# Performance work log

Measured on AMD Instinct MI355X. Metric: run time of the kernel, lower is better.

The kernel has to match this reference:

```python
import jax, jax.numpy as jnp
import numpy as np

N_NODES = 100000
N_EDGES = 1600000
N_GRAPHS = 1000


def _gcn_layer(x, W, b, row, col, dinv):
    # GCNConv with improved=True: A_hat = A + 2I, symmetric normalization.
    xw = x @ W  # [N, out]
    norm = dinv[row] * dinv[col]  # [E]
    agg = jax.ops.segment_sum(norm[:, None] * xw[row], col, num_segments=N_NODES)
    # self-loop contribution with fill weight 2.0
    agg = agg + (2.0 * dinv * dinv)[:, None] * xw
    return agg + b


def setup_inputs() -> dict:
    key = jax.random.key(0)
    ks = jax.random.split(key, 20)
    x = jax.random.normal(ks[0], (N_NODES, 336), dtype=jnp.float32)
    edge_index = jax.random.randint(ks[1], (2, N_EDGES), 0, N_NODES, dtype=jnp.int64)
    batch = jnp.sort(jax.random.randint(ks[2], (N_NODES,), 0, N_GRAPHS, dtype=jnp.int64))
    def lin(k, din, dout):
        s = 1.0 / np.sqrt(din)
        return jax.random.uniform(k, (din, dout), jnp.float32, -s, s)
    params = {
        'W1': lin(ks[3], 336, 100), 'b1': jnp.zeros((100,), jnp.float32),
        'W2': lin(ks[4], 100, 100), 'b2': jnp.zeros((100,), jnp.float32),
        'W3': lin(ks[5], 100, 100), 'b3': jnp.zeros((100,), jnp.float32),
        'W4': lin(ks[6], 100, 100), 'b4': jnp.zeros((100,), jnp.float32),
        'W5': lin(ks[7], 100, 100), 'b5': jnp.zeros((100,), jnp.float32),
        'Wl1': lin(ks[8], 100, 100), 'bl1': jnp.zeros((100,), jnp.float32),
        'Wl2': lin(ks[9], 100, 100), 'bl2': jnp.zeros((100,), jnp.float32),
        'Wl3': lin(ks[10], 100, 29), 'bl3': jnp.zeros((29,), jnp.float32),
    }
    return {'x': x, 'edge_index': edge_index, 'batch': batch, **params}


def reference(x, edge_index, batch, W1, b1, W2, b2, W3, b3, W4, b4, W5, b5,
              Wl1, bl1, Wl2, bl2, Wl3, bl3):
    row, col = edge_index[0], edge_index[1]
    # degree of A + 2I (edge weights are 1, self-loop weight 2)
    deg = jax.ops.segment_sum(jnp.ones((N_EDGES,), x.dtype), col, num_segments=N_NODES) + 2.0
    dinv = deg ** -0.5
    h = jax.nn.relu(_gcn_layer(x, W1, b1, row, col, dinv))
    h = jax.nn.relu(_gcn_layer(h, W2, b2, row, col, dinv))
    h = jax.nn.relu(_gcn_layer(h, W3, b3, row, col, dinv))
    h = jax.nn.relu(_gcn_layer(h, W4, b4, row, col, dinv))
    h = jax.nn.relu(_gcn_layer(h, W5, b5, row, col, dinv))
    # global mean pool over graphs
    sums = jax.ops.segment_sum(h, batch, num_segments=N_GRAPHS)
    counts = jax.ops.segment_sum(jnp.ones((N_NODES,), h.dtype), batch, num_segments=N_GRAPHS)
    pooled = sums / jnp.maximum(counts, 1.0)[:, None]
    g = jax.nn.relu(pooled @ Wl1 + bl1)
    g = jax.nn.relu(g @ Wl2 + bl2)
    return g @ Wl3 + bl3
```

## Files before the change

kernel.cpp:

```cpp
#include <hip/hip_runtime.h>
#include <hip/hip_fp16.h>
#include <stdint.h>

#define NN 100000
#define NE 1600000
#define NG 1000
#define LDA 112
#define LDX 128

#define NPART 8
#define PRANGE 12500
#define SGRID 2048
#define PSTRIDE 65536

typedef float f32x4 __attribute__((ext_vector_type(4)));
typedef _Float16 f16x8 __attribute__((ext_vector_type(8)));

__device__ __forceinline__ void load_lds16(const void* g, void* l) {
    __builtin_amdgcn_global_load_lds((const __attribute__((address_space(1))) unsigned int*)g,
                                     (__attribute__((address_space(3))) unsigned int*)l,
                                     16, 0, 0);
}

__global__ void k_deg(const int* __restrict__ col, int* __restrict__ degcnt) {
    int part = blockIdx.x & (NPART - 1);
    int pb = blockIdx.x >> 3;
    int lo = part * PRANGE, hi = lo + PRANGE;
    for (int e = pb * 256 + threadIdx.x; e < NE; e += PSTRIDE) {
        int c = col[e];
        if (c >= lo && c < hi) atomicAdd(&degcnt[c], 1);
    }
}

__global__ void k_scan1(const int* __restrict__ cnt, int* __restrict__ csum) {
    __shared__ int s[256];
    int i = blockIdx.x * 256 + threadIdx.x;
    s[threadIdx.x] = (i < NN) ? cnt[i] : 0;
    __syncthreads();
    for (int o = 128; o > 0; o >>= 1) {
        if (threadIdx.x < o) s[threadIdx.x] += s[threadIdx.x + o];
        __syncthreads();
    }
    if (threadIdx.x == 0) csum[blockIdx.x] = s[0];
}

__global__ void k_scan2(const int* __restrict__ csum, int* __restrict__ csum2, int nb) {
    __shared__ int s[512];
    int t = threadIdx.x;
    int v = (t < nb) ? csum[t] : 0;
    s[t] = v; __syncthreads();
    for (int o = 1; o < 512; o <<= 1) {
        int x = (t >= o) ? s[t - o] : 0;
        __syncthreads();
        s[t] += x;
        __syncthreads();
    }
    if (t < nb) csum2[t] = s[t] - v;
}

__global__ void k_scan3d(const int* __restrict__ cnt, const int* __restrict__ csum2,
                         int* __restrict__ indptr, float* __restrict__ dinv) {
    __shared__ int s[256];
    int t = threadIdx.x;
    int i = blockIdx.x * 256 + t;
    int v = (i < NN) ? cnt[i] : 0;
    s[t] = v; __syncthreads();
    for (int o = 1; o < 256; o <<= 1) {
        int x = (t >= o) ? s[t - o] : 0;
        __syncthreads();
        s[t] += x;
        __syncthreads();
    }
    if (i < NN) {
        indptr[i] = csum2[blockIdx.x] + s[t] - v;
        dinv[i] = 1.0f / sqrtf((float)v + 2.0f);
    }
    if (i == 0) indptr[NN] = NE;
}

__global__ void k_scatter(const int* __restrict__ row, const int* __restrict__ col,
                          const int* __restrict__ indptr,
                          int* __restrict__ fill, int* __restrict__ esrc) {
    int part = blockIdx.x & (NPART - 1);
    int pb = blockIdx.x >> 3;
    int lo = part * PRANGE, hi = lo + PRANGE;
    for (int e = pb * 256 + threadIdx.x; e < NE; e += PSTRIDE) {
        int c = col[e];
        int r = row[e];
        if (c >= lo && c < hi) {
            int pos = indptr[c] + atomicAdd(&fill[c], 1);
            esrc[pos] = r;
        }
    }
}

__global__ void k_gbounds(const int* __restrict__ batch, int* __restrict__ gstart) {
    int i = blockIdx.x * 256 + threadIdx.x;
    if (i >= NN) return;
    int b = batch[i];
    int pb = (i == 0) ? -1 : batch[i - 1];
    for (int g = pb + 1; g <= b; g++) gstart[g] = i;
    if (i == NN - 1) {
        for (int g = b + 1; g <= NG; g++) gstart[g] = NN;
    }
}

__global__ void k_convW(const float* __restrict__ W1, __half* __restrict__ w1h, __half* __restrict__ w1l,
                        const float* __restrict__ W2, __half* __restrict__ w2h, __half* __restrict__ w2l,
                        const float* __restrict__ W3, __half* __restrict__ w3h, __half* __restrict__ w3l,
                        const float* __restrict__ W4, __half* __restrict__ w4h, __half* __restrict__ w4l,
                        const float* __restrict__ W5, __half* __restrict__ w5h, __half* __restrict__ w5l) {
    int b = blockIdx.x, t = threadIdx.x;
    const float* W; __half *Wh, *Wl; int K, KCP, idx;
    if (b < 168) {
        W = W1; Wh = w1h; Wl = w1l; K = 336; KCP = 384; idx = b * 256 + t;
    } else {
        int li = (b - 168) / 56;
        int lb = (b - 168) % 56;
        const float* Ws[4] = {W2, W3, W4, W5};
        __half* Whs[4] = {w2h, w3h, w4h, w5h};
        __half* Wls[4] = {w2l, w3l, w4l, w5l};
        W = Ws[li]; Wh = Whs[li]; Wl = Wls[li]; K = 100; KCP = 128; idx = lb * 256 + t;
    }
    int n = idx / KCP, k = idx - n * KCP;
    float v = (n < 100 && k < K) ? W[k * 100 + n] : 0.f;
    __half hi = __float2half(v);
    __half lo = __float2half((v - __half2float(hi)) * 2048.f);
    int kc = k & 127;
    size_t so = (size_t)n * KCP + (k - kc) + (kc ^ ((n & 7) << 3));
    Wh[so] = hi;
    Wl[so] = lo;
}

__device__ __forceinline__ f16x8 cvt8(float4 v0, float4 v1) {
    __half2 p0 = __floats2half2_rn(v0.x, v0.y);
    __half2 p1 = __floats2half2_rn(v0.z, v0.w);
    __half2 p2 = __floats2half2_rn(v1.x, v1.y);
    __half2 p3 = __floats2half2_rn(v1.z, v1.w);
    union { uint4 u; f16x8 f; } c;
    c.u.x = __builtin_bit_cast(unsigned, p0);
    c.u.y = __builtin_bit_cast(unsigned, p1);
    c.u.z = __builtin_bit_cast(unsigned, p2);
    c.u.w = __builtin_bit_cast(unsigned, p3);
    return c.f;
}

__global__ __launch_bounds__(512, 4) void k_gemmX(const float* __restrict__ x,
                                                  const __half* __restrict__ Whi,
                                                  const __half* __restrict__ Wlo,
                                                  const float* __restrict__ dinv,
                                                  __half* __restrict__ out) {
    __shared__ __align__(16) __half Hs[112 * 128];
    __shared__ __align__(16) __half Ls[112 * 128];
    int t = threadIdx.x;
    int lane = t & 63, wv = t >> 6;
    int l15 = lane & 15, quad = lane >> 4;
    int rowbase = blockIdx.x * 128;
    int arow = rowbase + wv * 16 + l15;

    f32x4 acch[7], accl[7];
#pragma unroll
    for (int i = 0; i < 7; i++)
#pragma unroll
        for (int r = 0; r < 4; r++) { acch[i][r] = 0.f; accl[i][r] = 0.f; }

    int swz = (l15 & 7) << 4;

    for (int k0 = 0; k0 < 384; k0 += 128) {
        f16x8 a[4];
#pragma unroll
        for (int ks = 0; ks < 4; ks++) {
            int k = k0 + ks * 32 + quad * 8;
            float4 v0 = make_float4(0.f, 0.f, 0.f, 0.f), v1 = v0;
            if (arow < NN && k < 336) {
                const float* p = x + (size_t)arow * 336 + k;
                v0 = *(const float4*)p;
                v1 = *(const float4*)(p + 4);
            }
            a[ks] = cvt8(v0, v1);
        }
        if (k0) __syncthreads();
#pragma unroll
        for (int cch = 0; cch < 7; cch++) {
            int g = wv + cch * 8;
            int tb = (g >= 28);
            int o = (g - (tb ? 28 : 0)) * 1024 + lane * 16;
            int r = o >> 8, cc = o & 255;
            size_t src = (size_t)r * 768 + (size_t)(k0 * 2) + cc;
            if (!tb) load_lds16((const char*)Whi + src, (char*)Hs + o);
            else     load_lds16((const char*)Wlo + src, (char*)Ls + o);
        }
        __syncthreads();
#pragma unroll
        for (int ks = 0; ks < 4; ks++) {
            int cb = (ks * 64 + quad * 16) ^ swz;
#pragma unroll
            for (int tt = 0; tt < 7; tt++) {
                int ro = (tt * 16 + l15) * 256;
                f16x8 bh = *(const f16x8*)((const char*)Hs + ro + cb);
                f16x8 bl = *(const f16x8*)((const char*)Ls + ro + cb);
                acch[tt] = __builtin_amdgcn_mfma_f32_16x16x32_f16(a[ks], bh, acch[tt], 0, 0, 0);
                accl[tt] = __builtin_amdgcn_mfma_f32_16x16x32_f16(a[ks], bl, accl[tt], 0, 0, 0);
            }
        }
    }

    int gr0 = rowbase + wv * 16 + quad * 4;
    float dv[4];
#pragma unroll
    for (int reg = 0; reg < 4; reg++) dv[reg] = (gr0 + reg < NN) ? dinv[gr0 + reg] : 0.f;
#pragma unroll
    for (int tt = 0; tt < 7; tt++) {
        int n = tt * 16 + l15;
#pragma unroll
        for (int reg = 0; reg < 4; reg++) {
            int gr = gr0 + reg;
            if (gr < NN)
                out[(size_t)gr * LDX + n] =
                    __float2half(dv[reg] * (acch[tt][reg] + accl[tt][reg] * (1.f / 2048.f)));
        }
    }
    if (l15 < 8) {
#pragma unroll
        for (int reg = 0; reg < 4; reg++) {
            int gr = gr0 + reg;
            if (gr < NN) *(unsigned int*)(out + (size_t)gr * LDX + 112 + l15 * 2) = 0u;
        }
    }
}

__global__ __launch_bounds__(512, 4) void k_gemmH(const __half* __restrict__ act,
                                                  const __half* __restrict__ Whi,
                                                  const __half* __restrict__ Wlo,
                                                  const float* __restrict__ dinv,
                                                  __half* __restrict__ out) {
    __shared__ __align__(16) __half Hs[112 * 128];
    __shared__ __align__(16) __half Ls[112 * 128];
    int t = threadIdx.x;
    int lane = t & 63, wv = t >> 6;
    int l15 = lane & 15, quad = lane >> 4;
    int rowbase = blockIdx.x * 128;
    int ar = min(rowbase + wv * 16 + l15, NN - 1);

    const char* ap = (const char*)act + (size_t)ar * 256;
    f16x8 a[4];
#pragma unroll
    for (int ks = 0; ks < 4; ks++)
        a[ks] = *(const f16x8*)(ap + ks * 64 + quad * 16);

#pragma unroll
    for (int cch = 0; cch < 7; cch++) {
        int g = wv + cch * 8;
        int tb = (g >= 28);
        int o = (g - (tb ? 28 : 0)) * 1024 + lane * 16;
        if (!tb) load_lds16((const char*)Whi + o, (char*)Hs + o);
        else     load_lds16((const char*)Wlo + o, (char*)Ls + o);
    }

    f32x4 acch[7], accl[7];
#pragma unroll
    for (int i = 0; i < 7; i++)
#pragma unroll
        for (int r = 0; r < 4; r++) { acch[i][r] = 0.f; accl[i][r] = 0.f; }

    __syncthreads();
    int swz = (l15 & 7) << 4;
#pragma unroll
    for (int ks = 0; ks < 4; ks++) {
        int cb = (ks * 64 + quad * 16) ^ swz;
#pragma unroll
        for (int tt = 0; tt < 7; tt++) {
            int ro = (tt * 16 + l15) * 256;
            f16x8 bh = *(const f16x8*)((const char*)Hs + ro + cb);
            f16x8 bl = *(const f16x8*)((const char*)Ls + ro + cb);
            acch[tt] = __builtin_amdgcn_mfma_f32_16x16x32_f16(a[ks], bh, acch[tt], 0, 0, 0);
            accl[tt] = __builtin_amdgcn_mfma_f32_16x16x32_f16(a[ks], bl, accl[tt], 0, 0, 0);
        }
    }

    int gr0 = rowbase + wv * 16 + quad * 4;
    float dv[4];
#pragma unroll
    for (int reg = 0; reg < 4; reg++) dv[reg] = (gr0 + reg < NN) ? dinv[gr0 + reg] : 0.f;
#pragma unroll
    for (int tt = 0; tt < 7; tt++) {
        int n = tt * 16 + l15;
#pragma unroll
        for (int reg = 0; reg < 4; reg++) {
            int gr = gr0 + reg;
            if (gr < NN)
                out[(size_t)gr * LDX + n] =
                    __float2half(dv[reg] * (acch[tt][reg] + accl[tt][reg] * (1.f / 2048.f)));
        }
    }
    if (l15 < 8) {
#pragma unroll
        for (int reg = 0; reg < 4; reg++) {
            int gr = gr0 + reg;
            if (gr < NN) *(unsigned int*)(out + (size_t)gr * LDX + 112 + l15 * 2) = 0u;
        }
    }
}

__device__ __forceinline__ void agg_core(const __half* __restrict__ xs,
                                         const int* __restrict__ esrc,
                                         int beg, int end, int lane, int col,
                                         float& ax, float& ay) {
    ax = 0.f; ay = 0.f;
    for (int c = beg; c < end; c += 64) {
        int m = min(64, end - c);
        int se = 0;
        if (lane < m) se = esrc[c + lane];
        int j = 0;
        for (; j + 16 <= m; j += 16) {
            __half2 v[16];
#pragma unroll
            for (int u = 0; u < 16; u++) {
                int s = __builtin_amdgcn_readlane(se, j + u);
                v[u] = *(const __half2*)(xs + (size_t)s * LDX + col);
            }
#pragma unroll
            for (int u = 0; u < 16; u++) {
                float2 f = __half22float2(v[u]);
                ax += f.x; ay += f.y;
            }
        }
        for (; j + 8 <= m; j += 8) {
            __half2 v[8];
#pragma unroll
            for (int u = 0; u < 8; u++) {
                int s = __builtin_amdgcn_readlane(se, j + u);
                v[u] = *(const __half2*)(xs + (size_t)s * LDX + col);
            }
#pragma unroll
            for (int u = 0; u < 8; u++) {
                float2 f = __half22float2(v[u]);
                ax += f.x; ay += f.y;
            }
        }
        for (; j + 4 <= m; j += 4) {
            __half2 v[4];
#pragma unroll
            for (int u = 0; u < 4; u++) {
                int s = __builtin_amdgcn_readlane(se, j + u);
                v[u] = *(const __half2*)(xs + (size_t)s * LDX + col);
            }
#pragma unroll
            for (int u = 0; u < 4; u++) {
                float2 f = __half22float2(v[u]);
                ax += f.x; ay += f.y;
            }
        }
        for (; j < m; j++) {
            int s = __builtin_amdgcn_readlane(se, j);
            float2 f = __half22float2(*(const __half2*)(xs + (size_t)s * LDX + col));
            ax += f.x; ay += f.y;
        }
    }
}

__global__ __launch_bounds__(256) void k_aggS(const __half* __restrict__ xs,
                                              const int* __restrict__ indptr,
                                              const int* __restrict__ esrc,
                                              const float* __restrict__ dinv,
                                              const float* __restrict__ bias,
                                              __half* __restrict__ hh) {
    int wave = threadIdx.x >> 6;
    int lane = threadIdx.x & 63;
    int n = blockIdx.x * 4 + wave;
    if (n >= NN) return;
    int beg = indptr[n], end = indptr[n + 1];
    int col = (lane < 50) ? lane * 2 : 0;
    float ax, ay;
    agg_core(xs, esrc, beg, end, lane, col, ax, ay);
    if (lane < 50) {
        float di = dinv[n];
        float2 xv = __half22float2(*(const __half2*)(xs + (size_t)n * LDX + col));
        float2 bv = *(const float2*)(bias + lane * 2);
        float hx = fmaxf(di * (ax + 2.f * xv.x) + bv.x, 0.f);
        float hy = fmaxf(di * (ay + 2.f * xv.y) + bv.y, 0.f);
        *(__half2*)(hh + (size_t)n * LDX + col) = __floats2half2_rn(hx, hy);
    } else {
        int pc = 100 + (lane - 50) * 2;
        *(unsigned int*)(hh + (size_t)n * LDX + pc) = 0u;
    }
}

__global__ __launch_bounds__(256) void k_agg(const __half* __restrict__ xs,
                                             const int* __restrict__ indptr,
                                             const int* __restrict__ esrc,
                                             const float* __restrict__ dinv,
                                             const float* __restrict__ bias,
                                             float* __restrict__ hout) {
    int wave = threadIdx.x >> 6;
    int lane = threadIdx.x & 63;
    int n = blockIdx.x * 4 + wave;
    if (n >= NN) return;
    int beg = indptr[n], end = indptr[n + 1];
    int col = (lane < 50) ? lane * 2 : 0;
    float ax, ay;
    agg_core(xs, esrc, beg, end, lane, col, ax, ay);
    if (lane < 50) {
        float di = dinv[n];
        float2 xv = __half22float2(*(const __half2*)(xs + (size_t)n * LDX + col));
        float2 bv = *(const float2*)(bias + lane * 2);
        float2 r;
        r.x = fmaxf(di * (ax + 2.f * xv.x) + bv.x, 0.f);
        r.y = fmaxf(di * (ay + 2.f * xv.y) + bv.y, 0.f);
        *(float2*)(hout + (size_t)n * LDA + col) = r;
    }
}

__global__ __launch_bounds__(128) void k_pool(const float* __restrict__ h,
                                              const int* __restrict__ gstart,
                                              float* __restrict__ pooled) {
    int g = blockIdx.x, t = threadIdx.x;
    if (t >= 100) return;
    int st = gstart[g];
    int cnt = gstart[g + 1] - st;
    float s0 = 0.f, s1 = 0.f, s2 = 0.f, s3 = 0.f;
    float s4 = 0.f, s5 = 0.f, s6 = 0.f, s7 = 0.f;
    int i = 0;
    for (; i + 8 <= cnt; i += 8) {
        s0 += h[(size_t)(st + i) * LDA + t];
        s1 += h[(size_t)(st + i + 1) * LDA + t];
        s2 += h[(size_t)(st + i + 2) * LDA + t];
        s3 += h[(size_t)(st + i + 3) * LDA + t];
        s4 += h[(size_t)(st + i + 4) * LDA + t];
        s5 += h[(size_t)(st + i + 5) * LDA + t];
        s6 += h[(size_t)(st + i + 6) * LDA + t];
        s7 += h[(size_t)(st + i + 7) * LDA + t];
    }
    for (; i < cnt; i++) s0 += h[(size_t)(st + i) * LDA + t];
    float s = ((s0 + s1) + (s2 + s3)) + ((s4 + s5) + (s6 + s7));
    pooled[g * 100 + t] = s / (float)(cnt > 0 ? cnt : 1);
}

__global__ void k_mlp(const float* __restrict__ pooled,
                      const float* __restrict__ Wl1, const float* __restrict__ bl1,
                      const float* __restrict__ Wl2, const float* __restrict__ bl2,
                      const float* __restrict__ Wl3, const float* __restrict__ bl3,
                      float* __restrict__ out) {
    __shared__ float p[100], q[100];
    int g = blockIdx.x, t = threadIdx.x;
    if (t < 100) p[t] = pooled[g * 100 + t];
    __syncthreads();
    float s1 = 0.f;
    if (t < 100) {
        s1 = bl1[t];
        for (int k = 0; k < 100; k++) s1 += p[k] * Wl1[k * 100 + t];
        s1 = fmaxf(s1, 0.f);
    }
    __syncthreads();
    if (t < 100) q[t] = s1;
    __syncthreads();
    float s2 = 0.f;
    if (t < 100) {
        s2 = bl2[t];
        for (int k = 0; k < 100; k++) s2 += q[k] * Wl2[k * 100 + t];
        s2 = fmaxf(s2, 0.f);
    }
    __syncthreads();
    if (t < 100) p[t] = s2;
    __syncthreads();
    if (t < 29) {
        float s3 = bl3[t];
        for (int k = 0; k < 100; k++) s3 += p[k] * Wl3[k * 29 + t];
        out[g * 29 + t] = s3;
    }
}

extern "C" void kernel_launch(void* const* d_in, const int* in_sizes, int n_in,
                              void* d_out, int out_size, void* d_ws, size_t ws_size,
                              hipStream_t stream) {
    const float* x     = (const float*)d_in[0];
    const int*   ei    = (const int*)d_in[1];
    const int*   batch = (const int*)d_in[2];
    const float* W1 = (const float*)d_in[3];  const float* b1 = (const float*)d_in[4];
    const float* W2 = (const float*)d_in[5];  const float* b2 = (const float*)d_in[6];
    const float* W3 = (const float*)d_in[7];  const float* b3 = (const float*)d_in[8];
    const float* W4 = (const float*)d_in[9];  const float* b4 = (const float*)d_in[10];
    const float* W5 = (const float*)d_in[11]; const float* b5 = (const float*)d_in[12];
    const float* Wl1 = (const float*)d_in[13]; const float* bl1 = (const float*)d_in[14];
    const float* Wl2 = (const float*)d_in[15]; const float* bl2 = (const float*)d_in[16];
    const float* Wl3 = (const float*)d_in[17]; const float* bl3 = (const float*)d_in[18];
    float* out = (float*)d_out;

    const int* row = ei;
    const int* col = ei + NE;

    uintptr_t base = (uintptr_t)d_ws;
    auto alloc = [&](size_t bytes) -> void* {
        void* p = (void*)base;
        base += (bytes + 255) & ~(size_t)255;
        return p;
    };
    int*   cnts   = (int*)alloc((size_t)(2 * NN) * 4);
    int*   degcnt = cnts;
    int*   fill   = cnts + NN;
    float* dinv   = (float*)alloc(NN * 4);
    int*   indptr = (int*)alloc((NN + 1) * 4);
    int*   csum   = (int*)alloc(512 * 4);
    int*   csum2  = (int*)alloc(512 * 4);
    int*   gstart = (int*)alloc((NG + 1) * 4);
    int*   esrc   = (int*)alloc((size_t)NE * 4);
    __half* xsh   = (__half*)alloc((size_t)NN * LDX * 2);
    __half* hh    = (__half*)alloc((size_t)NN * LDX * 2);
    float* h      = (float*)alloc((size_t)NN * LDA * 4);
    float* pooled = (float*)alloc((size_t)NG * 100 * 4);
    __half* w1hi = (__half*)alloc((size_t)112 * 384 * 2);
    __half* w1lo = (__half*)alloc((size_t)112 * 384 * 2);
    __half* w2hi = (__half*)alloc((size_t)112 * 128 * 2);
    __half* w2lo = (__half*)alloc((size_t)112 * 128 * 2);
    __half* w3hi = (__half*)alloc((size_t)112 * 128 * 2);
    __half* w3lo = (__half*)alloc((size_t)112 * 128 * 2);
    __half* w4hi = (__half*)alloc((size_t)112 * 128 * 2);
    __half* w4lo = (__half*)alloc((size_t)112 * 128 * 2);
    __half* w5hi = (__half*)alloc((size_t)112 * 128 * 2);
    __half* w5lo = (__half*)alloc((size_t)112 * 128 * 2);

    hipMemsetAsync(cnts, 0, (size_t)(2 * NN) * 4, stream);

    const int NB = (NN + 255) / 256;
    k_deg<<<SGRID, 256, 0, stream>>>(col, degcnt);
    k_scan1<<<NB, 256, 0, stream>>>(degcnt, csum);
    k_scan2<<<1, 512, 0, stream>>>(csum, csum2, NB);
    k_scan3d<<<NB, 256, 0, stream>>>(degcnt, csum2, indptr, dinv);
    k_scatter<<<SGRID, 256, 0, stream>>>(row, col, indptr, fill, esrc);
    k_gbounds<<<NB, 256, 0, stream>>>(batch, gstart);
    k_convW<<<392, 256, 0, stream>>>(W1, w1hi, w1lo, W2, w2hi, w2lo,
                                     W3, w3hi, w3lo, W4, w4hi, w4lo,
                                     W5, w5hi, w5lo);

    const int GEMM_GRID = (NN + 127) / 128;
    const int AGG_GRID = (NN + 3) / 4;

    k_gemmX<<<GEMM_GRID, 512, 0, stream>>>(x, w1hi, w1lo, dinv, xsh);
    k_aggS<<<AGG_GRID, 256, 0, stream>>>(xsh, indptr, esrc, dinv, b1, hh);
    k_gemmH<<<GEMM_GRID, 512, 0, stream>>>(hh, w2hi, w2lo, dinv, xsh);
    k_aggS<<<AGG_GRID, 256, 0, stream>>>(xsh, indptr, esrc, dinv, b2, hh);
    k_gemmH<<<GEMM_GRID, 512, 0, stream>>>(hh, w3hi, w3lo, dinv, xsh);
    k_aggS<<<AGG_GRID, 256, 0, stream>>>(xsh, indptr, esrc, dinv, b3, hh);
    k_gemmH<<<GEMM_GRID, 512, 0, stream>>>(hh, w4hi, w4lo, dinv, xsh);
    k_aggS<<<AGG_GRID, 256, 0, stream>>>(xsh, indptr, esrc, dinv, b4, hh);
    k_gemmH<<<GEMM_GRID, 512, 0, stream>>>(hh, w5hi, w5lo, dinv, xsh);
    k_agg<<<AGG_GRID, 256, 0, stream>>>(xsh, indptr, esrc, dinv, b5, h);

    k_pool<<<NG, 128, 0, stream>>>(h, gstart, pooled);
    k_mlp<<<NG, 128, 0, stream>>>(pooled, Wl1, bl1, Wl2, bl2, Wl3, bl3, out);
}
```

Baseline: 828.4 us.

## Double-buffer X GEMM weight/activation loads and widen aggregation gather unroll

The first-layer GEMM now double-buffers the LDS weight tiles and prefetches the next K-chunk of x into registers while MFMAs run on the current chunk. It uses explicit waitcnt and barriers, and lowers the occupancy hint to 2 blocks per CU to fit the doubled LDS. Separately, the edge aggregation gather gains a 32-wide unrolled path so more independent loads are in flight at once. Risks are higher register pressure and lower occupancy in both kernels.

```diff
diff --git a/kernel.cpp b/kernel.cpp
--- a/kernel.cpp
+++ b/kernel.cpp
@@ -145,18 +145,20 @@
     return c.f;
 }
 
-__global__ __launch_bounds__(512, 4) void k_gemmX(const float* __restrict__ x,
+__global__ __launch_bounds__(512, 2) void k_gemmX(const float* __restrict__ x,
                                                   const __half* __restrict__ Whi,
                                                   const __half* __restrict__ Wlo,
                                                   const float* __restrict__ dinv,
                                                   __half* __restrict__ out) {
-    __shared__ __align__(16) __half Hs[112 * 128];
-    __shared__ __align__(16) __half Ls[112 * 128];
+    __shared__ __align__(16) __half Hs[2][112 * 128];
+    __shared__ __align__(16) __half Ls[2][112 * 128];
     int t = threadIdx.x;
     int lane = t & 63, wv = t >> 6;
     int l15 = lane & 15, quad = lane >> 4;
     int rowbase = blockIdx.x * 128;
     int arow = rowbase + wv * 16 + l15;
+    bool arok = arow < NN;
+    const float* xp = x + (size_t)arow * 336;
 
     f32x4 acch[7], accl[7];
 #pragma unroll
@@ -165,21 +167,9 @@
         for (int r = 0; r < 4; r++) { acch[i][r] = 0.f; accl[i][r] = 0.f; }
 
     int swz = (l15 & 7) << 4;
-
-    for (int k0 = 0; k0 < 384; k0 += 128) {
-        f16x8 a[4];
-#pragma unroll
-        for (int ks = 0; ks < 4; ks++) {
-            int k = k0 + ks * 32 + quad * 8;
-            float4 v0 = make_float4(0.f, 0.f, 0.f, 0.f), v1 = v0;
-            if (arow < NN && k < 336) {
-                const float* p = x + (size_t)arow * 336 + k;
-                v0 = *(const float4*)p;
-                v1 = *(const float4*)(p + 4);
-            }
-            a[ks] = cvt8(v0, v1);
-        }
-        if (k0) __syncthreads();
+    float4 araw[8];
+
+    auto stage = [&](int buf, int k0) {
 #pragma unroll
         for (int cch = 0; cch < 7; cch++) {
             int g = wv + cch * 8;
@@ -187,22 +177,55 @@
             int o = (g - (tb ? 28 : 0)) * 1024 + lane * 16;
             int r = o >> 8, cc = o & 255;
             size_t src = (size_t)r * 768 + (size_t)(k0 * 2) + cc;
-            if (!tb) load_lds16((const char*)Whi + src, (char*)Hs + o);
-            else     load_lds16((const char*)Wlo + src, (char*)Ls + o);
-        }
-        __syncthreads();
+            if (!tb) load_lds16((const char*)Whi + src, (char*)Hs[buf] + o);
+            else     load_lds16((const char*)Wlo + src, (char*)Ls[buf] + o);
+        }
+    };
+    auto aload = [&](int k0) {
+#pragma unroll
+        for (int ks = 0; ks < 4; ks++) {
+            int k = k0 + ks * 32 + quad * 8;
+            float4 v0 = make_float4(0.f, 0.f, 0.f, 0.f), v1 = v0;
+            if (arok && k < 336) {
+                v0 = *(const float4*)(xp + k);
+                v1 = *(const float4*)(xp + k + 4);
+            }
+            araw[ks * 2] = v0;
+            araw[ks * 2 + 1] = v1;
+        }
+    };
+
+    stage(0, 0);
+    aload(0);
+
+#pragma unroll
+    for (int tch = 0; tch < 3; tch++) {
+        asm volatile("s_waitcnt vmcnt(0)" ::: "memory");
+        f16x8 a[4];
+#pragma unroll
+        for (int ks = 0; ks < 4; ks++) a[ks] = cvt8(araw[ks * 2], araw[ks * 2 + 1]);
+        __builtin_amdgcn_s_barrier();
+        __builtin_amdgcn_sched_barrier(0);
+        if (tch < 2) {
+            aload((tch + 1) * 128);
+            stage((tch + 1) & 1, (tch + 1) * 128);
+        }
+        const char* HB = (const char*)Hs[tch & 1];
+        const char* LB = (const char*)Ls[tch & 1];
 #pragma unroll
         for (int ks = 0; ks < 4; ks++) {
             int cb = (ks * 64 + quad * 16) ^ swz;
 #pragma unroll
             for (int tt = 0; tt < 7; tt++) {
                 int ro = (tt * 16 + l15) * 256;
-                f16x8 bh = *(const f16x8*)((const char*)Hs + ro + cb);
-                f16x8 bl = *(const f16x8*)((const char*)Ls + ro + cb);
+                f16x8 bh = *(const f16x8*)(HB + ro + cb);
+                f16x8 bl = *(const f16x8*)(LB + ro + cb);
                 acch[tt] = __builtin_amdgcn_mfma_f32_16x16x32_f16(a[ks], bh, acch[tt], 0, 0, 0);
                 accl[tt] = __builtin_amdgcn_mfma_f32_16x16x32_f16(a[ks], bl, accl[tt], 0, 0, 0);
             }
         }
+        __builtin_amdgcn_sched_barrier(0);
+        __builtin_amdgcn_s_barrier();
     }
 
     int gr0 = rowbase + wv * 16 + quad * 4;
@@ -312,6 +335,19 @@
         int se = 0;
         if (lane < m) se = esrc[c + lane];
         int j = 0;
+        for (; j + 32 <= m; j += 32) {
+            __half2 v[32];
+#pragma unroll
+            for (int u = 0; u < 32; u++) {
+                int s = __builtin_amdgcn_readlane(se, j + u);
+                v[u] = *(const __half2*)(xs + (size_t)s * LDX + col);
+            }
+#pragma unroll
+            for (int u = 0; u < 32; u++) {
+                float2 f = __half22float2(v[u]);
+                ax += f.x; ay += f.y;
+            }
+        }
         for (; j + 16 <= m; j += 16) {
             __half2 v[16];
 #pragma unroll
```

New measurement: 835.5 us. About the same (+0.9%).
